# Kernel tuning notes

Hardware: AMD Instinct MI355X
Metric: run time of the kernel (lower is better)

The kernel has to match this reference:

```python
import jax, jax.numpy as jnp
import numpy as np
import math

D_MODEL = 1024
N_HEADS = 16
D_HEAD = D_MODEL // N_HEADS  # 64, even (required for RoPE)
MAX_LEN = 1024


def _rope_cache(max_len, d_head, dtype=jnp.float32):
    half = d_head // 2
    inv_freq = jnp.exp(jnp.arange(half, dtype=dtype) * (-math.log(10000.0) / half))
    angles = jnp.arange(max_len, dtype=dtype)[:, None] * inv_freq[None, :]  # [max_len, half]
    return jnp.cos(angles), jnp.sin(angles)


def _apply_rope(t, cos, sin):
    # t: [B, H, L, D]; rotate-by-halves variant (cat of halves, not interleave)
    L = t.shape[2]
    half = t.shape[-1] // 2
    c = cos[:L, :half][None, None, :, :].astype(t.dtype)
    s = sin[:L, :half][None, None, :, :].astype(t.dtype)
    t1, t2 = t[..., :half], t[..., half:]
    return jnp.concatenate([t1 * c - t2 * s, t1 * s + t2 * c], axis=-1)


def setup_inputs() -> dict:
    key = jax.random.key(0)
    ks = jax.random.split(key, 11)
    B, L = 4, 1024
    std = 1.0 / math.sqrt(D_MODEL)
    return {
        "queries": jax.random.normal(ks[0], (B, L, D_MODEL), jnp.float32),
        "keys": jax.random.normal(ks[1], (B, L, D_MODEL), jnp.float32),
        "values": jax.random.normal(ks[2], (B, L, D_MODEL), jnp.float32),
        "Wq": jax.random.normal(ks[3], (D_MODEL, D_MODEL), jnp.float32) * std,
        "bq": jnp.zeros((D_MODEL,), jnp.float32),
        "Wk": jax.random.normal(ks[4], (D_MODEL, D_MODEL), jnp.float32) * std,
        "bk": jnp.zeros((D_MODEL,), jnp.float32),
        "Wv": jax.random.normal(ks[5], (D_MODEL, D_MODEL), jnp.float32) * std,
        "bv": jnp.zeros((D_MODEL,), jnp.float32),
        "Wo": jax.random.normal(ks[6], (D_MODEL, D_MODEL), jnp.float32) * std,
        "bo": jnp.zeros((D_MODEL,), jnp.float32),
    }


def reference(queries, keys, values, Wq, bq, Wk, bk, Wv, bv, Wo, bo):
    B, L, _ = queries.shape
    S = keys.shape[1]
    H, Dh = N_HEADS, D_HEAD
    cos, sin = _rope_cache(MAX_LEN, Dh, queries.dtype)

    q = (queries @ Wq + bq).reshape(B, L, H, Dh).transpose(0, 2, 1, 3)  # [B,H,L,Dh]
    k = (keys @ Wk + bk).reshape(B, S, H, Dh).transpose(0, 2, 1, 3)
    v = (values @ Wv + bv).reshape(B, S, H, Dh).transpose(0, 2, 1, 3)

    q = _apply_rope(q, cos, sin)
    k = _apply_rope(k, cos, sin)

    scores = jnp.einsum('bhid,bhjd->bhij', q, k) / math.sqrt(Dh)
    attn = jax.nn.softmax(scores, axis=-1)  # dropout is identity in eval
    out = jnp.einsum('bhij,bhjd->bhid', attn, v)  # [B,H,L,Dh]
    out = out.transpose(0, 2, 1, 3).reshape(B, L, H * Dh)
    return out @ Wo + bo
```

## Files before the change

### kernel.cpp

```cpp
#include <hip/hip_runtime.h>
#include <math.h>

#define BB 4
#define LL 1024
#define HH 16
#define DH 64
#define DM 1024
#define MM (BB * LL)

typedef short bf16x8 __attribute__((ext_vector_type(8)));
typedef float f32x4  __attribute__((ext_vector_type(4)));
typedef unsigned short u16x4 __attribute__((ext_vector_type(4)));
typedef unsigned int   u32x2 __attribute__((ext_vector_type(2)));

__device__ __forceinline__ unsigned short f2bf(float x) {
    union { float f; unsigned u; } v; v.f = x;
    unsigned r = v.u + 0x7fff + ((v.u >> 16) & 1);
    return (unsigned short)(r >> 16);
}

__device__ __forceinline__ unsigned int fbits(float x) {
    union { float f; unsigned u; } v; v.f = x; return v.u;
}

__device__ __forceinline__ void gl2lds16(const unsigned short* g, unsigned short* l) {
    __builtin_amdgcn_global_load_lds(
        (const __attribute__((address_space(1))) unsigned int*)g,
        (__attribute__((address_space(3))) unsigned int*)l, 16, 0, 0);
}

__device__ __forceinline__ void tile_map64(int n, int& tM, int& tN) {
    tM = ((n >> 7) * 8 + (n & 7)) * 128;
    tN = ((n >> 3) & 15) * 64;
}

__global__ __launch_bounds__(256) void prep_kernel(
    const float* __restrict__ i0, const float* __restrict__ i1, const float* __restrict__ i2,
    unsigned short* __restrict__ o0, unsigned short* __restrict__ o1, unsigned short* __restrict__ o2,
    const float* __restrict__ w0, const float* __restrict__ w1,
    const float* __restrict__ w2, const float* __restrict__ w3,
    unsigned short* __restrict__ t0, unsigned short* __restrict__ t1,
    unsigned short* __restrict__ t2, unsigned short* __restrict__ t3,
    float* __restrict__ ct, float* __restrict__ st)
{
    const int z = blockIdx.z;
    const int bid = blockIdx.x, tid = threadIdx.x;

    if (z < 3) {
        const float* in = (z == 0) ? i0 : (z == 1) ? i1 : i2;
        unsigned short* out = (z == 0) ? o0 : (z == 1) ? o1 : o2;
        #pragma unroll
        for (int it = 0; it < 4; ++it) {
            size_t i = ((size_t)(it * 1024 + bid) * 256 + tid) * 4;
            float4 f = *(const float4*)(in + i);
            u16x4 r;
            r.x = f2bf(f.x); r.y = f2bf(f.y); r.z = f2bf(f.z); r.w = f2bf(f.w);
            *(u16x4*)(out + i) = r;
        }
    } else if (z == 3) {
        int idx = bid * 256 + tid;
        if (idx < LL * 32) {
            int l = idx >> 5, d = idx & 31;
            const float coef = -0.28782313662425583f;
            float ang = (float)l * expf((float)d * coef);
            float s, c;
            sincosf(ang, &s, &c);
            ct[idx] = c;
            st[idx] = s;
        }
    } else {
        const int w = z - 4;
        const float* in = (w == 0) ? w0 : (w == 1) ? w1 : (w == 2) ? w2 : w3;
        unsigned short* out = (w == 0) ? t0 : (w == 1) ? t1 : (w == 2) ? t2 : t3;
        __shared__ float tile[32][33];
        int tx = tid & 31, ty = tid >> 5;
        int c0 = (bid & 31) * 32, r0 = (bid >> 5) * 32;
        #pragma unroll
        for (int j = 0; j < 32; j += 8)
            tile[ty + j][tx] = in[(size_t)(r0 + ty + j) * 1024 + c0 + tx];
        __syncthreads();
        #pragma unroll
        for (int j = 0; j < 32; j += 8)
            out[(size_t)(c0 + ty + j) * 1024 + r0 + tx] = f2bf(tile[tx][ty + j]);
    }
}

__device__ __forceinline__ void gemm128x64_sb(
    const unsigned short* __restrict__ A, const unsigned short* __restrict__ Bt,
    unsigned short* As, unsigned short* Bs, int tM, int tN, f32x4 (&acc)[4][2])
{
    const int tid  = threadIdx.x;
    const int wave = tid >> 6, lane = tid & 63;
    const int g = lane >> 4, lm = lane & 15;
    const int wm = wave >> 1, wn = wave & 1;
    const int lr = lane >> 3, lk = lane & 7;
    const int kbl = lk ^ lr;

    for (int kt = 0; kt < 16; ++kt) {
        const int k0 = kt * 64;
        if (kt) __syncthreads();
        #pragma unroll
        for (int it = 0; it < 4; ++it) {
            int rbase = wave * 32 + it * 8;
            int r = rbase + lr;
            gl2lds16(A + (size_t)(tM + r) * 1024 + k0 + kbl * 8, As + rbase * 64);
        }
        #pragma unroll
        for (int it = 0; it < 2; ++it) {
            int rbase = wave * 16 + it * 8;
            int r = rbase + lr;
            gl2lds16(Bt + (size_t)(tN + r) * 1024 + k0 + kbl * 8, Bs + rbase * 64);
        }
        __syncthreads();

        #pragma unroll
        for (int kk = 0; kk < 2; ++kk) {
            bf16x8 a[4], b[2];
            const int sw = ((kk * 4 + g) ^ (lm & 7)) * 8;
            #pragma unroll
            for (int mt = 0; mt < 4; ++mt)
                a[mt] = *(const bf16x8*)&As[(wm * 64 + mt * 16 + lm) * 64 + sw];
            #pragma unroll
            for (int nt = 0; nt < 2; ++nt)
                b[nt] = *(const bf16x8*)&Bs[(wn * 16 + nt * 32 + lm) * 64 + sw];
            #pragma unroll
            for (int mt = 0; mt < 4; ++mt)
                #pragma unroll
                for (int nt = 0; nt < 2; ++nt)
                    acc[mt][nt] = __builtin_amdgcn_mfma_f32_16x16x32_bf16(
                        a[mt], b[nt], acc[mt][nt], 0, 0, 0);
        }
    }
}

__global__ __launch_bounds__(256) void gemm_qkv_kernel(
    const unsigned short* __restrict__ Aq, const unsigned short* __restrict__ Ak,
    const unsigned short* __restrict__ Av,
    const unsigned short* __restrict__ Wqt, const unsigned short* __restrict__ Wkt,
    const unsigned short* __restrict__ Wvt,
    const float* __restrict__ bq, const float* __restrict__ bk, const float* __restrict__ bv,
    const float* __restrict__ ct, const float* __restrict__ st,
    unsigned short* __restrict__ oq, unsigned short* __restrict__ ok,
    unsigned short* __restrict__ vt)
{
    __shared__ __align__(16) unsigned short As[128 * 64];
    __shared__ __align__(16) unsigned short Bs[64 * 64];

    const int z = blockIdx.z;
    const unsigned short* A  = (z == 0) ? Aq  : (z == 1) ? Ak  : Av;
    const unsigned short* Bt = (z == 0) ? Wqt : (z == 1) ? Wkt : Wvt;
    const float* bias        = (z == 0) ? bq  : (z == 1) ? bk  : bv;

    int tM, tN;
    tile_map64(blockIdx.x, tM, tN);
    f32x4 acc[4][2] = {};
    gemm128x64_sb(A, Bt, As, Bs, tM, tN, acc);

    const int wave = threadIdx.x >> 6, lane = threadIdx.x & 63;
    const int g = lane >> 4, lm = lane & 15;
    const int wm = wave >> 1, wn = wave & 1;

    const int h = tN >> 6;
    float bvv[2];
    #pragma unroll
    for (int nt = 0; nt < 2; ++nt) bvv[nt] = bias[tN + wn * 16 + nt * 32 + lm];

    if (z == 2) {
        #pragma unroll
        for (int mt = 0; mt < 4; ++mt) {
            int row0 = tM + wm * 64 + mt * 16 + g * 4;
            int b = row0 >> 10, l0 = row0 & 1023;
            #pragma unroll
            for (int nt = 0; nt < 2; ++nt) {
                int dloc = wn * 16 + nt * 32 + lm;
                u16x4 p4;
                #pragma unroll
                for (int r = 0; r < 4; ++r)
                    p4[r] = f2bf(acc[mt][nt][r] + bvv[nt]);
                *(u16x4*)(vt + (((size_t)(b * HH + h) * DH + dloc) << 10) + l0) = p4;
            }
        }
    } else {
        unsigned short* out = (z == 0) ? oq : ok;
        const float sc = (z == 0) ? 0.125f * 1.4426950408889634f : 1.0f;
        const int dlo = wn * 16 + lm;
        #pragma unroll
        for (int mt = 0; mt < 4; ++mt)
            #pragma unroll
            for (int r = 0; r < 4; ++r) {
                int row = tM + wm * 64 + mt * 16 + g * 4 + r;
                int b = row >> 10, l = row & 1023;
                float c = ct[l * 32 + dlo];
                float s = st[l * 32 + dlo];
                unsigned short* orow = out + ((size_t)(b * HH + h) * LL + l) * DH;
                float t1 = acc[mt][0][r] + bvv[0];
                float t2 = acc[mt][1][r] + bvv[1];
                orow[dlo]      = f2bf((t1 * c - t2 * s) * sc);
                orow[dlo + 32] = f2bf((t1 * s + t2 * c) * sc);
            }
    }
}

__global__ __launch_bounds__(256) void gemm_out_kernel(
    const unsigned short* __restrict__ A, const unsigned short* __restrict__ Bt,
    const float* __restrict__ bias, float* __restrict__ C)
{
    __shared__ __align__(16) unsigned short As[128 * 64];
    __shared__ __align__(16) unsigned short Bs[64 * 64];

    int tM, tN;
    tile_map64(blockIdx.x, tM, tN);
    f32x4 acc[4][2] = {};
    gemm128x64_sb(A, Bt, As, Bs, tM, tN, acc);

    const int wave = threadIdx.x >> 6, lane = threadIdx.x & 63;
    const int g = lane >> 4, lm = lane & 15;
    const int wm = wave >> 1, wn = wave & 1;

    float bvv[2];
    #pragma unroll
    for (int nt = 0; nt < 2; ++nt) bvv[nt] = bias[tN + wn * 16 + nt * 32 + lm];
    #pragma unroll
    for (int mt = 0; mt < 4; ++mt)
        #pragma unroll
        for (int r = 0; r < 4; ++r) {
            int row = tM + wm * 64 + mt * 16 + g * 4 + r;
            float* crow = C + (size_t)row * DM + tN;
            #pragma unroll
            for (int nt = 0; nt < 2; ++nt)
                crow[wn * 16 + nt * 32 + lm] = acc[mt][nt][r] + bvv[nt];
        }
}

#define PSTR 72

__global__ __launch_bounds__(256) void attn_mfma_kernel(
    const unsigned short* __restrict__ q, const unsigned short* __restrict__ k,
    const unsigned short* __restrict__ vt, unsigned short* __restrict__ ctx)
{
    __shared__ __align__(16) unsigned short Ks[64 * 64];
    __shared__ __align__(16) unsigned short Vs[64 * 64];
    __shared__ __align__(16) unsigned short Pb[4][16 * PSTR];

    const int tid  = threadIdx.x;
    const int wave = tid >> 6, lane = tid & 63;
    const int g = lane >> 4, lm = lane & 15;
    const int lr = lane >> 3, lk = lane & 7;
    const int kbl = lk ^ lr;
    const int n = blockIdx.x;
    const int bh = n & 63;
    const int qbase = (n >> 6) * 64;

    const unsigned short* qg  = q  + (size_t)(bh * LL + qbase) * DH;
    const unsigned short* kg  = k  + (size_t)bh * LL * DH;
    const unsigned short* vtg = vt + (size_t)bh * DH * LL;

    bf16x8 aq[2];
    {
        const unsigned short* qrow = qg + (wave * 16 + lm) * DH;
        aq[0] = *(const bf16x8*)(qrow + g * 8);
        aq[1] = *(const bf16x8*)(qrow + 32 + g * 8);
    }

    f32x4 acc[4] = {};
    float lsum = 0.f;

    for (int kt = 0; kt < 16; ++kt) {
        if (kt) __syncthreads();
        #pragma unroll
        for (int it = 0; it < 2; ++it) {
            int rbase = wave * 16 + it * 8;
            int r = rbase + lr;
            gl2lds16(kg  + (size_t)(kt * 64 + r) * DH + kbl * 8, Ks + rbase * 64);
            gl2lds16(vtg + (size_t)r * LL + kt * 64 + kbl * 8,  Vs + rbase * 64);
        }
        __syncthreads();

        f32x4 s[4] = {};
        #pragma unroll
        for (int kk = 0; kk < 2; ++kk) {
            const int sw = ((kk * 4 + g) ^ (lm & 7)) * 8;
            #pragma unroll
            for (int t = 0; t < 4; ++t) {
                bf16x8 ak = *(const bf16x8*)&Ks[(t * 16 + lm) * 64 + sw];
                s[t] = __builtin_amdgcn_mfma_f32_16x16x32_bf16(ak, aq[kk], s[t], 0, 0, 0);
            }
        }

        #pragma unroll
        for (int t = 0; t < 4; ++t) {
            float p0 = exp2f(s[t][0]), p1 = exp2f(s[t][1]);
            float p2 = exp2f(s[t][2]), p3 = exp2f(s[t][3]);
            lsum += (p0 + p1) + (p2 + p3);
            u32x2 pk;
            pk[0] = __builtin_amdgcn_perm(fbits(p1), fbits(p0), 0x07060302u);
            pk[1] = __builtin_amdgcn_perm(fbits(p3), fbits(p2), 0x07060302u);
            *(u32x2*)&Pb[wave][lm * PSTR + t * 16 + g * 4] = pk;
        }

        #pragma unroll
        for (int kk = 0; kk < 2; ++kk) {
            const int sw = ((kk * 4 + g) ^ (lm & 7)) * 8;
            bf16x8 ap = *(const bf16x8*)&Pb[wave][lm * PSTR + kk * 32 + g * 8];
            #pragma unroll
            for (int dt = 0; dt < 4; ++dt) {
                bf16x8 bv = *(const bf16x8*)&Vs[(dt * 16 + lm) * 64 + sw];
                acc[dt] = __builtin_amdgcn_mfma_f32_16x16x32_bf16(ap, bv, acc[dt], 0, 0, 0);
            }
        }
    }

    float ts = lsum;
    ts += __shfl_xor(ts, 16, 64);
    ts += __shfl_xor(ts, 32, 64);

    int b = bh >> 4, h = bh & 15;
    #pragma unroll
    for (int r = 0; r < 4; ++r) {
        float inv = 1.f / __shfl(ts, g * 4 + r, 64);
        int qrow = qbase + wave * 16 + g * 4 + r;
        unsigned short* orow = ctx + (size_t)(b * LL + qrow) * DM + h * DH;
        #pragma unroll
        for (int dt = 0; dt < 4; ++dt)
            orow[dt * 16 + lm] = f2bf(acc[dt][r] * inv);
    }
}

extern "C" void kernel_launch(void* const* d_in, const int* in_sizes, int n_in,
                              void* d_out, int out_size, void* d_ws, size_t ws_size,
                              hipStream_t stream) {
    const float* queries = (const float*)d_in[0];
    const float* keys    = (const float*)d_in[1];
    const float* values  = (const float*)d_in[2];
    const float* Wq = (const float*)d_in[3];
    const float* bq = (const float*)d_in[4];
    const float* Wk = (const float*)d_in[5];
    const float* bk = (const float*)d_in[6];
    const float* Wv = (const float*)d_in[7];
    const float* bv = (const float*)d_in[8];
    const float* Wo = (const float*)d_in[9];
    const float* bo = (const float*)d_in[10];
    float* out = (float*)d_out;

    unsigned short* qb   = (unsigned short*)d_ws;
    unsigned short* kb_  = qb  + (size_t)MM * DM;
    unsigned short* vb_  = kb_ + (size_t)MM * DM;
    unsigned short* Wqt  = vb_ + (size_t)MM * DM;
    unsigned short* Wkt  = Wqt + (size_t)DM * DM;
    unsigned short* Wvt  = Wkt + (size_t)DM * DM;
    unsigned short* Wot  = Wvt + (size_t)DM * DM;
    unsigned short* q_ws = Wot + (size_t)DM * DM;
    unsigned short* k_ws = q_ws + (size_t)MM * DM;
    unsigned short* vt   = k_ws + (size_t)MM * DM;
    unsigned short* ctx  = vt   + (size_t)MM * DM;
    float* rope_cos = (float*)ctx;
    float* rope_sin = rope_cos + LL * 32;

    prep_kernel<<<dim3(1024, 1, 8), 256, 0, stream>>>(
        queries, keys, values, qb, kb_, vb_,
        Wq, Wk, Wv, Wo, Wqt, Wkt, Wvt, Wot, rope_cos, rope_sin);
    gemm_qkv_kernel<<<dim3(512, 1, 3), 256, 0, stream>>>(
        qb, kb_, vb_, Wqt, Wkt, Wvt, bq, bk, bv, rope_cos, rope_sin,
        q_ws, k_ws, vt);
    attn_mfma_kernel<<<dim3(LL / 64 * BB * HH), 256, 0, stream>>>(
        q_ws, k_ws, vt, ctx);
    gemm_out_kernel<<<dim3(512), 256, 0, stream>>>(
        ctx, Wot, bo, out);
}
```

Baseline: 207.9 us.

## Split attention work across wave pairs with 512-thread blocks

The attention kernel now runs 8 waves per block instead of 4. Each pair of waves shares 16 query rows: each wave computes scores for half of the key tile and accumulates half of the head dimension. The P tile is exchanged through LDS behind an extra block barrier, and row sums are combined through a small shared array. This raises per-block parallelism and shrinks per-wave register use, at the cost of one more __syncthreads per key tile and duplicated Q loads within each pair.

```diff
diff --git a/kernel.cpp b/kernel.cpp
--- a/kernel.cpp
+++ b/kernel.cpp
@@ -234,16 +234,18 @@
 
 #define PSTR 72
 
-__global__ __launch_bounds__(256) void attn_mfma_kernel(
+__global__ __launch_bounds__(512) void attn_mfma_kernel(
     const unsigned short* __restrict__ q, const unsigned short* __restrict__ k,
     const unsigned short* __restrict__ vt, unsigned short* __restrict__ ctx)
 {
     __shared__ __align__(16) unsigned short Ks[64 * 64];
     __shared__ __align__(16) unsigned short Vs[64 * 64];
     __shared__ __align__(16) unsigned short Pb[4][16 * PSTR];
+    __shared__ float Sm[4][2][16];
 
     const int tid  = threadIdx.x;
     const int wave = tid >> 6, lane = tid & 63;
+    const int pair = wave >> 1, half = wave & 1;
     const int g = lane >> 4, lm = lane & 15;
     const int lr = lane >> 3, lk = lane & 7;
     const int kbl = lk ^ lr;
@@ -257,54 +259,53 @@
 
     bf16x8 aq[2];
     {
-        const unsigned short* qrow = qg + (wave * 16 + lm) * DH;
+        const unsigned short* qrow = qg + (pair * 16 + lm) * DH;
         aq[0] = *(const bf16x8*)(qrow + g * 8);
         aq[1] = *(const bf16x8*)(qrow + 32 + g * 8);
     }
 
-    f32x4 acc[4] = {};
+    f32x4 acc[2] = {};
     float lsum = 0.f;
 
     for (int kt = 0; kt < 16; ++kt) {
         if (kt) __syncthreads();
-        #pragma unroll
-        for (int it = 0; it < 2; ++it) {
-            int rbase = wave * 16 + it * 8;
-            int r = rbase + lr;
-            gl2lds16(kg  + (size_t)(kt * 64 + r) * DH + kbl * 8, Ks + rbase * 64);
-            gl2lds16(vtg + (size_t)r * LL + kt * 64 + kbl * 8,  Vs + rbase * 64);
+        {
+            int r = wave * 8 + lr;
+            gl2lds16(kg  + (size_t)(kt * 64 + r) * DH + kbl * 8, Ks + wave * 8 * 64);
+            gl2lds16(vtg + (size_t)r * LL + kt * 64 + kbl * 8,  Vs + wave * 8 * 64);
         }
         __syncthreads();
 
-        f32x4 s[4] = {};
+        f32x4 s[2] = {};
         #pragma unroll
         for (int kk = 0; kk < 2; ++kk) {
             const int sw = ((kk * 4 + g) ^ (lm & 7)) * 8;
             #pragma unroll
-            for (int t = 0; t < 4; ++t) {
-                bf16x8 ak = *(const bf16x8*)&Ks[(t * 16 + lm) * 64 + sw];
+            for (int t = 0; t < 2; ++t) {
+                bf16x8 ak = *(const bf16x8*)&Ks[(half * 32 + t * 16 + lm) * 64 + sw];
                 s[t] = __builtin_amdgcn_mfma_f32_16x16x32_bf16(ak, aq[kk], s[t], 0, 0, 0);
             }
         }
 
         #pragma unroll
-        for (int t = 0; t < 4; ++t) {
+        for (int t = 0; t < 2; ++t) {
             float p0 = exp2f(s[t][0]), p1 = exp2f(s[t][1]);
             float p2 = exp2f(s[t][2]), p3 = exp2f(s[t][3]);
             lsum += (p0 + p1) + (p2 + p3);
             u32x2 pk;
             pk[0] = __builtin_amdgcn_perm(fbits(p1), fbits(p0), 0x07060302u);
             pk[1] = __builtin_amdgcn_perm(fbits(p3), fbits(p2), 0x07060302u);
-            *(u32x2*)&Pb[wave][lm * PSTR + t * 16 + g * 4] = pk;
-        }
+            *(u32x2*)&Pb[pair][lm * PSTR + half * 32 + t * 16 + g * 4] = pk;
+        }
+        __syncthreads();
 
         #pragma unroll
         for (int kk = 0; kk < 2; ++kk) {
             const int sw = ((kk * 4 + g) ^ (lm & 7)) * 8;
-            bf16x8 ap = *(const bf16x8*)&Pb[wave][lm * PSTR + kk * 32 + g * 8];
-            #pragma unroll
-            for (int dt = 0; dt < 4; ++dt) {
-                bf16x8 bv = *(const bf16x8*)&Vs[(dt * 16 + lm) * 64 + sw];
+            bf16x8 ap = *(const bf16x8*)&Pb[pair][lm * PSTR + kk * 32 + g * 8];
+            #pragma unroll
+            for (int dt = 0; dt < 2; ++dt) {
+                bf16x8 bv = *(const bf16x8*)&Vs[(half * 32 + dt * 16 + lm) * 64 + sw];
                 acc[dt] = __builtin_amdgcn_mfma_f32_16x16x32_bf16(ap, bv, acc[dt], 0, 0, 0);
             }
         }
@@ -313,16 +314,19 @@
     float ts = lsum;
     ts += __shfl_xor(ts, 16, 64);
     ts += __shfl_xor(ts, 32, 64);
+    if (lane < 16) Sm[pair][half][lane] = ts;
+    __syncthreads();
 
     int b = bh >> 4, h = bh & 15;
     #pragma unroll
     for (int r = 0; r < 4; ++r) {
-        float inv = 1.f / __shfl(ts, g * 4 + r, 64);
-        int qrow = qbase + wave * 16 + g * 4 + r;
+        int m = g * 4 + r;
+        float inv = 1.f / (Sm[pair][0][m] + Sm[pair][1][m]);
+        int qrow = qbase + pair * 16 + m;
         unsigned short* orow = ctx + (size_t)(b * LL + qrow) * DM + h * DH;
         #pragma unroll
-        for (int dt = 0; dt < 4; ++dt)
-            orow[dt * 16 + lm] = f2bf(acc[dt][r] * inv);
+        for (int dt = 0; dt < 2; ++dt)
+            orow[half * 32 + dt * 16 + lm] = f2bf(acc[dt][r] * inv);
     }
 }
 
@@ -362,7 +366,7 @@
     gemm_qkv_kernel<<<dim3(512, 1, 3), 256, 0, stream>>>(
         qb, kb_, vb_, Wqt, Wkt, Wvt, bq, bk, bv, rope_cos, rope_sin,
         q_ws, k_ws, vt);
-    attn_mfma_kernel<<<dim3(LL / 64 * BB * HH), 256, 0, stream>>>(
+    attn_mfma_kernel<<<dim3(LL / 64 * BB * HH), 512, 0, stream>>>(
         q_ws, k_ws, vt, ctx);
     gemm_out_kernel<<<dim3(512), 256, 0, stream>>>(
         ctx, Wot, bo, out);
```

Measured after the change: 204.3 us, median of 2. Within noise of the previous version (-1.7%).
